# Kernel optimization log

Measured on AMD Instinct MI355X. Metric: run time of the kernel, lower is better.

The kernel has to match this reference:

```python
import jax, jax.numpy as jnp
import numpy as np

N, CIN, COUT, H, W = 32, 256, 256, 56, 56

def setup_inputs() -> dict:
    key = jax.random.key(0)
    k1, k2, k3 = jax.random.split(key, 3)
    x = jax.random.normal(k1, (N, CIN, H, W), dtype=jnp.float32)
    weight = jax.random.normal(k2, (COUT, CIN, 3, 3), dtype=jnp.float32) * 0.05
    bias = jax.random.normal(k3, (COUT,), dtype=jnp.float32)
    return {"x": x, "weight": weight, "bias": bias}

def reference(x, weight, bias):
    # 3x3 conv, stride=1, padding=1 (SAME), fused bias + ReLU.
    # Winograd F(2x2,3x3) is mathematically identical to direct conv.
    y = jax.lax.conv_general_dilated(
        x, weight,
        window_strides=(1, 1),
        padding=((1, 1), (1, 1)),
        dimension_numbers=("NCHW", "OIHW", "NCHW"),
    )
    return jax.nn.relu(y + bias[None, :, None, None])
```

## Files before the change

### kernel.cpp

```cpp
#include <hip/hip_runtime.h>


#define GLOBAL_AS __attribute__((address_space(1)))
#define LDS_AS __attribute__((address_space(3)))

typedef __attribute__((ext_vector_type(8))) short short8;
typedef __attribute__((ext_vector_type(4))) float f32x4;
typedef __attribute__((ext_vector_type(4))) unsigned int u32x4;

#define CIN   256
#define HWS   3136
#define PTOT  100352
#define KTOT  2304
#define IMGP  3364
#define XTOFF 1310720
#define XTBYTES ((size_t)32 * IMGP * 512)
#define WSNEED (XTOFF + XTBYTES)

__device__ __forceinline__ unsigned short f2bf(float f) {
  unsigned u = __builtin_bit_cast(unsigned, f);
  return (unsigned short)((u + 0x7fffu + ((u >> 16) & 1u)) >> 16);
}

__global__ void wcvt_kernel(const float* __restrict__ w, unsigned char* __restrict__ ws) {
  int o = blockIdx.x * 256 + threadIdx.x;
  int co = o / KTOT;
  int r  = o - co * KTOT;
  int s  = r >> 6;
  int c  = r & 63;
  int cq = s / 9;
  int tap = s - cq * 9;
  ((unsigned short*)ws)[o] = f2bf(w[co * KTOT + (cq * 64 + c) * 9 + tap]);
}

__global__ __launch_bounds__(256) void xcvt_kernel(const float* __restrict__ x,
                                                   unsigned char* __restrict__ ws) {
  __shared__ float lt[64 * 257];
  const int pg0 = blockIdx.x * 64;
  const int n   = pg0 / HWS;
  const int pi0 = pg0 - n * HWS;
  const int t   = threadIdx.x;
  {
    const int px = t & 63;
    const int cg = t >> 6;
    const float* xb = x + ((size_t)n * 256) * HWS + pi0 + px;
#pragma unroll 8
    for (int i = 0; i < 64; ++i) {
      const int c = i * 4 + cg;
      lt[px * 257 + c] = xb[(size_t)c * HWS];
    }
  }
  __syncthreads();
  {
    const int slot = t & 31;
    const int pxw  = t >> 5;
    unsigned char* xt = ws + XTOFF;
#pragma unroll
    for (int i = 0; i < 8; ++i) {
      const int p  = i * 8 + pxw;
      const int pi = pi0 + p;
      const int h  = pi / 56;
      const int wcol = pi - h * 56;
      const size_t gran = (size_t)n * IMGP + (h + 1) * 58 + (wcol + 1);
      const float* r = &lt[p * 257 + slot * 8];
      u32x4 v;
#pragma unroll
      for (int j = 0; j < 4; ++j)
        v[j] = (unsigned)f2bf(r[2 * j]) | ((unsigned)f2bf(r[2 * j + 1]) << 16);
      *(u32x4*)(xt + gran * 512 + slot * 16) = v;
    }
  }
}

#define DTAP(tp) (((((tp) / 3) - 1) * 58 + ((tp) % 3) - 1) * 512)

__global__ __launch_bounds__(256, 2) void conv_kernel(
    const unsigned char* __restrict__ ws, const float* __restrict__ bias,
    float* __restrict__ out) {
  __shared__ __align__(16) unsigned char smem[65536];

  const unsigned char* wf = ws;
  const unsigned char* xt = ws + XTOFF;

  const int bid = blockIdx.x;
  const int sw  = (bid & 7) * 196 + (bid >> 3);
  const int co0 = (sw & 1) * 128;
  const int p0  = (sw >> 1) * 128;

  const int t    = threadIdx.x;
  const int lane = t & 63;
  const int wave = t >> 6;
  const int wm   = wave & 1;
  const int wn   = wave >> 1;
  const int rl   = lane & 15;
  const int kq   = lane >> 4;
  const int l7   = lane & 7;
  const int l8   = lane >> 3;

  const unsigned chanoff = (unsigned)((l7 * 16) ^ ((l8 & 7) << 4));

  const unsigned char* aP[4];
  const unsigned char* bP[4];
#pragma unroll
  for (int i = 0; i < 4; ++i) {
    const int row = wave * 32 + i * 8 + l8;
    aP[i] = wf + (size_t)(co0 + row) * 4608 + chanoff;
    const int pg = p0 + row;
    const int n  = pg / HWS;
    const int pi = pg - n * HWS;
    const int h  = pi / 56;
    const int wc = pi - h * 56;
    bP[i] = xt + ((size_t)n * IMGP + (h + 1) * 58 + (wc + 1)) * 512 + chanoff;
  }
  const unsigned ldsA = (unsigned)(wave * 4096);

  const unsigned krd0 = (unsigned)((kq * 16) ^ (l7 << 4));
  const unsigned krd1 = (unsigned)((kq * 16 + 64) ^ (l7 << 4));
  const unsigned char* pA0 = smem + (wm * 64 + rl) * 128 + krd0;
  const unsigned char* pA1 = smem + (wm * 64 + rl) * 128 + krd1;
  const unsigned char* pB0 = smem + 16384 + (wn * 64 + rl) * 128 + krd0;
  const unsigned char* pB1 = smem + 16384 + (wn * 64 + rl) * 128 + krd1;

  f32x4 acc[4][4];
  const f32x4 zero4 = {0.f, 0.f, 0.f, 0.f};
#pragma unroll
  for (int mi = 0; mi < 4; ++mi)
#pragma unroll
    for (int ni = 0; ni < 4; ++ni) acc[mi][ni] = zero4;

#define STAGE(DB, AOFF, BD)                                                   \
  {                                                                           \
    _Pragma("unroll") for (int i_ = 0; i_ < 4; ++i_)                          \
        __builtin_amdgcn_global_load_lds(                                     \
            (const GLOBAL_AS unsigned int*)(aP[i_] + (AOFF)),                 \
            (LDS_AS unsigned int*)(smem + (DB)*32768 + ldsA + i_ * 1024),     \
            16, 0, 0);                                                        \
    _Pragma("unroll") for (int i_ = 0; i_ < 4; ++i_)                          \
        __builtin_amdgcn_global_load_lds(                                     \
            (const GLOBAL_AS unsigned int*)(bP[i_] + (BD)),                   \
            (LDS_AS unsigned int*)(smem + (DB)*32768 + 16384 + ldsA +         \
                                   i_ * 1024),                                \
            16, 0, 0);                                                        \
  }

#define COMP(BUF)                                                             \
  {                                                                           \
    short8 av[4], bv[4];                                                      \
    _Pragma("unroll") for (int mi = 0; mi < 4; ++mi)                          \
        av[mi] = *(const short8*)(pA0 + (BUF)*32768 + mi * 2048);             \
    _Pragma("unroll") for (int ni = 0; ni < 4; ++ni)                          \
        bv[ni] = *(const short8*)(pB0 + (BUF)*32768 + ni * 2048);             \
    _Pragma("unroll") for (int mi = 0; mi < 4; ++mi)                          \
      _Pragma("unroll") for (int ni = 0; ni < 4; ++ni)                        \
          acc[mi][ni] = __builtin_amdgcn_mfma_f32_16x16x32_bf16(              \
              av[mi], bv[ni], acc[mi][ni], 0, 0, 0);                          \
    _Pragma("unroll") for (int mi = 0; mi < 4; ++mi)                          \
        av[mi] = *(const short8*)(pA1 + (BUF)*32768 + mi * 2048);             \
    _Pragma("unroll") for (int ni = 0; ni < 4; ++ni)                          \
        bv[ni] = *(const short8*)(pB1 + (BUF)*32768 + ni * 2048);             \
    _Pragma("unroll") for (int mi = 0; mi < 4; ++mi)                          \
      _Pragma("unroll") for (int ni = 0; ni < 4; ++ni)                        \
          acc[mi][ni] = __builtin_amdgcn_mfma_f32_16x16x32_bf16(              \
              av[mi], bv[ni], acc[mi][ni], 0, 0, 0);                          \
  }

#define STEPJ(J)                                                              \
  STAGE(((J) + 1) & 1, ((J) + 1) * 128,                                       \
        DTAP((((J) + 1) % 9)) + (((J) + 1) / 9) * 128);                       \
  COMP((J)&1);                                                                \
  __syncthreads();

  STAGE(0, 0, DTAP(0))
  __syncthreads();

#pragma unroll 1
  for (int gg = 0; gg < 2; ++gg) {
    STEPJ(0) STEPJ(1) STEPJ(2) STEPJ(3) STEPJ(4) STEPJ(5) STEPJ(6) STEPJ(7)
    STEPJ(8) STEPJ(9) STEPJ(10) STEPJ(11) STEPJ(12) STEPJ(13) STEPJ(14)
    STEPJ(15) STEPJ(16)
    if (gg == 0) {
#pragma unroll
      for (int i = 0; i < 4; ++i) {
        aP[i] += 2304;
        bP[i] += 256;
      }
      STAGE(0, 0, DTAP(0))
    }
    COMP(1)
    __syncthreads();
  }
#undef STEPJ
#undef COMP
#undef STAGE

#pragma unroll
  for (int mi = 0; mi < 4; ++mi) {
    const int row = co0 + wm * 64 + mi * 16 + kq * 4;
    float br[4];
#pragma unroll
    for (int j = 0; j < 4; ++j) br[j] = bias[row + j];
#pragma unroll
    for (int ni = 0; ni < 4; ++ni) {
      const int pgb = p0 + wn * 64 + ni * 16;
      const int n   = pgb / HWS;
      const int pib = pgb - n * HWS;
#pragma unroll
      for (int j = 0; j < 4; ++j) {
        float v = acc[mi][ni][j] + br[j];
        out[(size_t)(n * 256 + row + j) * HWS + pib + rl] = fmaxf(v, 0.f);
      }
    }
  }
}

__global__ void naive_kernel(const float* __restrict__ x, const float* __restrict__ w,
                             const float* __restrict__ bias, float* __restrict__ out) {
  int idx = blockIdx.x * 256 + threadIdx.x;
  if (idx >= 32 * 256 * HWS) return;
  int n  = idx / (256 * HWS);
  int r  = idx - n * 256 * HWS;
  int co = r / HWS;
  int p  = r - co * HWS;
  int h = p / 56, ww = p - h * 56;
  float s = bias[co];
  const float* xb = x + (size_t)n * 256 * HWS;
  const float* wbp = w + (size_t)co * KTOT;
  for (int ci = 0; ci < 256; ++ci) {
    const float* xc = xb + (size_t)ci * HWS;
    const float* wc = wbp + ci * 9;
    for (int kh = 0; kh < 3; ++kh) {
      int hh = h + kh - 1;
      if ((unsigned)hh >= 56u) continue;
      for (int kw = 0; kw < 3; ++kw) {
        int w2 = ww + kw - 1;
        if ((unsigned)w2 >= 56u) continue;
        s += xc[hh * 56 + w2] * wc[kh * 3 + kw];
      }
    }
  }
  out[idx] = fmaxf(s, 0.f);
}

extern "C" void kernel_launch(void* const* d_in, const int* in_sizes, int n_in,
                              void* d_out, int out_size, void* d_ws, size_t ws_size,
                              hipStream_t stream) {
  const float* x    = (const float*)d_in[0];
  const float* w    = (const float*)d_in[1];
  const float* bias = (const float*)d_in[2];
  float* out        = (float*)d_out;

  if (ws_size < WSNEED) {
    hipLaunchKernelGGL(naive_kernel, dim3((32 * 256 * HWS + 255) / 256), dim3(256),
                       0, stream, x, w, bias, out);
    return;
  }
  unsigned char* ws = (unsigned char*)d_ws;
  hipMemsetAsync(ws + XTOFF, 0, XTBYTES, stream);
  hipLaunchKernelGGL(wcvt_kernel, dim3(2304), dim3(256), 0, stream, w, ws);
  hipLaunchKernelGGL(xcvt_kernel, dim3(PTOT / 64), dim3(256), 0, stream, x, ws);
  hipLaunchKernelGGL(conv_kernel, dim3(1568), dim3(256), 0, stream, ws, bias, out);
}
```

Measured before the change: 170.8 us.

## Use 32x32x16 bf16 MFMA tiles and zero only padding halo in workspace

The conv GEMM inner loop moves from a 4x4 grid of 16x16x32 MFMAs per wave to a 2x2 grid of 32x32x16 MFMAs. This cuts the LDS fragment reads per MFMA and the instruction count, and the LDS addressing and epilogue mapping are rewritten to match. The full-workspace memset of the padded input buffer is replaced by extra blocks in the weight-convert kernel that zero only the border pixels, which removes about 55MB of memset traffic and a separate launch. The risk is that the new LDS read pattern brings bank conflicts, and the epilogue now loads bias per element.

New measurement: 174.5 us. 2.2% more time.

```diff
diff --git a/kernel.cpp b/kernel.cpp
--- a/kernel.cpp
+++ b/kernel.cpp
@@ -6,6 +6,7 @@
 
 typedef __attribute__((ext_vector_type(8))) short short8;
 typedef __attribute__((ext_vector_type(4))) float f32x4;
+typedef __attribute__((ext_vector_type(16))) float f32x16;
 typedef __attribute__((ext_vector_type(4))) unsigned int u32x4;
 
 #define CIN   256
@@ -23,7 +24,25 @@
 }
 
 __global__ void wcvt_kernel(const float* __restrict__ w, unsigned char* __restrict__ ws) {
-  int o = blockIdx.x * 256 + threadIdx.x;
+  const int bid = blockIdx.x;
+  if (bid >= 2304) {
+    const unsigned i = (unsigned)(bid - 2304) * 256 + threadIdx.x;
+    if (i < 233472u) {
+      const int slot = i & 31;
+      const int g    = i >> 5;
+      const int img  = g / 228;
+      const int hg   = g - img * 228;
+      int r, c;
+      if (hg < 58)        { r = 0;            c = hg; }
+      else if (hg < 116)  { r = 57;           c = hg - 58; }
+      else if (hg < 172)  { r = hg - 116 + 1; c = 0; }
+      else                { r = hg - 172 + 1; c = 57; }
+      const u32x4 z = {0u, 0u, 0u, 0u};
+      *(u32x4*)(ws + XTOFF + ((size_t)img * IMGP + r * 58 + c) * 512 + slot * 16) = z;
+    }
+    return;
+  }
+  int o = bid * 256 + threadIdx.x;
   int co = o / KTOT;
   int r  = o - co * KTOT;
   int s  = r >> 6;
@@ -92,8 +111,8 @@
   const int wave = t >> 6;
   const int wm   = wave & 1;
   const int wn   = wave >> 1;
-  const int rl   = lane & 15;
-  const int kq   = lane >> 4;
+  const int l31  = lane & 31;
+  const int hi   = lane >> 5;
   const int l7   = lane & 7;
   const int l8   = lane >> 3;
 
@@ -114,19 +133,22 @@
   }
   const unsigned ldsA = (unsigned)(wave * 4096);
 
-  const unsigned krd0 = (unsigned)((kq * 16) ^ (l7 << 4));
-  const unsigned krd1 = (unsigned)((kq * 16 + 64) ^ (l7 << 4));
-  const unsigned char* pA0 = smem + (wm * 64 + rl) * 128 + krd0;
-  const unsigned char* pA1 = smem + (wm * 64 + rl) * 128 + krd1;
-  const unsigned char* pB0 = smem + 16384 + (wn * 64 + rl) * 128 + krd0;
-  const unsigned char* pB1 = smem + 16384 + (wn * 64 + rl) * 128 + krd1;
-
-  f32x4 acc[4][4];
-  const f32x4 zero4 = {0.f, 0.f, 0.f, 0.f};
-#pragma unroll
-  for (int mi = 0; mi < 4; ++mi)
-#pragma unroll
-    for (int ni = 0; ni < 4; ++ni) acc[mi][ni] = zero4;
+  const unsigned char* pA[4];
+  const unsigned char* pB[4];
+#pragma unroll
+  for (int ks = 0; ks < 4; ++ks) {
+    const unsigned krd = (unsigned)(((ks * 2 + hi) ^ l7) * 16);
+    pA[ks] = smem + wm * 8192 + l31 * 128 + krd;
+    pB[ks] = smem + 16384 + wn * 8192 + l31 * 128 + krd;
+  }
+
+  f32x16 acc[2][2];
+#pragma unroll
+  for (int mi = 0; mi < 2; ++mi)
+#pragma unroll
+    for (int ni = 0; ni < 2; ++ni)
+#pragma unroll
+      for (int j = 0; j < 16; ++j) acc[mi][ni][j] = 0.f;
 
 #define STAGE(DB, AOFF, BD)                                                   \
   {                                                                           \
@@ -145,23 +167,17 @@
 
 #define COMP(BUF)                                                             \
   {                                                                           \
-    short8 av[4], bv[4];                                                      \
-    _Pragma("unroll") for (int mi = 0; mi < 4; ++mi)                          \
-        av[mi] = *(const short8*)(pA0 + (BUF)*32768 + mi * 2048);             \
-    _Pragma("unroll") for (int ni = 0; ni < 4; ++ni)                          \
-        bv[ni] = *(const short8*)(pB0 + (BUF)*32768 + ni * 2048);             \
-    _Pragma("unroll") for (int mi = 0; mi < 4; ++mi)                          \
-      _Pragma("unroll") for (int ni = 0; ni < 4; ++ni)                        \
-          acc[mi][ni] = __builtin_amdgcn_mfma_f32_16x16x32_bf16(              \
-              av[mi], bv[ni], acc[mi][ni], 0, 0, 0);                          \
-    _Pragma("unroll") for (int mi = 0; mi < 4; ++mi)                          \
-        av[mi] = *(const short8*)(pA1 + (BUF)*32768 + mi * 2048);             \
-    _Pragma("unroll") for (int ni = 0; ni < 4; ++ni)                          \
-        bv[ni] = *(const short8*)(pB1 + (BUF)*32768 + ni * 2048);             \
-    _Pragma("unroll") for (int mi = 0; mi < 4; ++mi)                          \
-      _Pragma("unroll") for (int ni = 0; ni < 4; ++ni)                        \
-          acc[mi][ni] = __builtin_amdgcn_mfma_f32_16x16x32_bf16(              \
-              av[mi], bv[ni], acc[mi][ni], 0, 0, 0);                          \
+    _Pragma("unroll") for (int ks = 0; ks < 4; ++ks) {                        \
+      short8 av[2], bv[2];                                                    \
+      _Pragma("unroll") for (int mi = 0; mi < 2; ++mi)                        \
+          av[mi] = *(const short8*)(pA[ks] + (BUF)*32768 + mi * 4096);        \
+      _Pragma("unroll") for (int ni = 0; ni < 2; ++ni)                        \
+          bv[ni] = *(const short8*)(pB[ks] + (BUF)*32768 + ni * 4096);        \
+      _Pragma("unroll") for (int mi = 0; mi < 2; ++mi)                        \
+        _Pragma("unroll") for (int ni = 0; ni < 2; ++ni)                      \
+            acc[mi][ni] = __builtin_amdgcn_mfma_f32_32x32x16_bf16(            \
+                av[mi], bv[ni], acc[mi][ni], 0, 0, 0);                        \
+    }                                                                         \
   }
 
 #define STEPJ(J)                                                              \
@@ -194,20 +210,17 @@
 #undef STAGE
 
 #pragma unroll
-  for (int mi = 0; mi < 4; ++mi) {
-    const int row = co0 + wm * 64 + mi * 16 + kq * 4;
-    float br[4];
-#pragma unroll
-    for (int j = 0; j < 4; ++j) br[j] = bias[row + j];
-#pragma unroll
-    for (int ni = 0; ni < 4; ++ni) {
-      const int pgb = p0 + wn * 64 + ni * 16;
+  for (int mi = 0; mi < 2; ++mi) {
+#pragma unroll
+    for (int ni = 0; ni < 2; ++ni) {
+      const int pgb = p0 + wn * 64 + ni * 32;
       const int n   = pgb / HWS;
       const int pib = pgb - n * HWS;
 #pragma unroll
-      for (int j = 0; j < 4; ++j) {
-        float v = acc[mi][ni][j] + br[j];
-        out[(size_t)(n * 256 + row + j) * HWS + pib + rl] = fmaxf(v, 0.f);
+      for (int j = 0; j < 16; ++j) {
+        const int row = co0 + wm * 64 + mi * 32 + (j & 3) + 8 * (j >> 2) + 4 * hi;
+        float v = acc[mi][ni][j] + bias[row];
+        out[(size_t)(n * 256 + row) * HWS + pib + l31] = fmaxf(v, 0.f);
       }
     }
   }
@@ -255,8 +268,7 @@
     return;
   }
   unsigned char* ws = (unsigned char*)d_ws;
-  hipMemsetAsync(ws + XTOFF, 0, XTBYTES, stream);
-  hipLaunchKernelGGL(wcvt_kernel, dim3(2304), dim3(256), 0, stream, w, ws);
+  hipLaunchKernelGGL(wcvt_kernel, dim3(3216), dim3(256), 0, stream, w, ws);
   hipLaunchKernelGGL(xcvt_kernel, dim3(PTOT / 64), dim3(256), 0, stream, x, ws);
   hipLaunchKernelGGL(conv_kernel, dim3(1568), dim3(256), 0, stream, ws, bias, out);
 }
```
